# Kernel tuning notes

Measured on AMD Instinct MI355X. Metric: run time of the kernel, lower is better.

Reference implementation:

```python
import jax, jax.numpy as jnp
import numpy as np

B, H1, H2, D, V1 = 4, 512, 640, 640, 1025  # V1 = vocab_size + 1 (blank)
T, U = 256, 128


def setup_inputs() -> dict:
    key = jax.random.key(0)
    ks = jax.random.split(key, 8)
    s = lambda fan_in: 1.0 / np.sqrt(fan_in)
    return {
        "encoder_outputs": jax.random.normal(ks[0], (B, H1, T), jnp.float32),
        "predictor_outputs": jax.random.normal(ks[1], (B, H2, U), jnp.float32),
        # Linear weights stored as [in, out]
        "W_enc": jax.random.uniform(ks[2], (H1, D), jnp.float32, -s(H1), s(H1)),
        "b_enc": jax.random.uniform(ks[3], (D,), jnp.float32, -s(H1), s(H1)),
        "W_pred": jax.random.uniform(ks[4], (H2, D), jnp.float32, -s(H2), s(H2)),
        "b_pred": jax.random.uniform(ks[5], (D,), jnp.float32, -s(H2), s(H2)),
        "W_out": jax.random.uniform(ks[6], (D, V1), jnp.float32, -s(D), s(D)),
        "b_out": jax.random.uniform(ks[7], (V1,), jnp.float32, -s(D), s(D)),
    }


def reference(encoder_outputs, predictor_outputs, W_enc, b_enc, W_pred, b_pred, W_out, b_out):
    # transpose(1,2): [B,H1,T] -> [B,T,H1], [B,H2,U] -> [B,U,H2], fused into einsum
    f = jnp.einsum("bht,hd->btd", encoder_outputs, W_enc) + b_enc   # [B,T,D]
    g = jnp.einsum("bhu,hd->bud", predictor_outputs, W_pred) + b_pred  # [B,U,D]
    h = jax.nn.relu(f[:, :, None, :] + g[:, None, :, :])            # [B,T,U,D]
    logits = jnp.einsum("btud,dv->btuv", h, W_out) + b_out          # [B,T,U,V+1]
    return jax.nn.log_softmax(logits, axis=-1)
```

## Files before the change

### kernel.cpp

```cpp
#include <hip/hip_runtime.h>
#include <hip/hip_bf16.h>

#define Bb 4
#define Tt 256
#define Uu 128
#define H1 512
#define H2 640
#define Dd 640
#define V1c 1025

typedef __bf16 bf16x8 __attribute__((ext_vector_type(8)));
typedef unsigned short ushort8 __attribute__((ext_vector_type(8)));
typedef unsigned short ushort4v __attribute__((ext_vector_type(4)));
typedef float floatx4 __attribute__((ext_vector_type(4)));

static __device__ __forceinline__ unsigned short f2bf(float x) {
    union { float f; unsigned u; } a; a.f = x;
    unsigned r = a.u + 0x7fffu + ((a.u >> 16) & 1u);
    return (unsigned short)(r >> 16);
}
static __device__ __forceinline__ float bf2f(unsigned short x) {
    union { unsigned u; float f; } a; a.u = ((unsigned)x) << 16; return a.f;
}

__global__ __launch_bounds__(640) void prep(const float* __restrict__ enc,
                                            const float* __restrict__ Wenc,
                                            const float* __restrict__ benc,
                                            float* __restrict__ f,
                                            const float* __restrict__ pred,
                                            const float* __restrict__ Wpred,
                                            const float* __restrict__ bpred,
                                            float* __restrict__ g,
                                            const float* __restrict__ Wout,
                                            unsigned short* __restrict__ Wb2,
                                            float* __restrict__ wtail) {
    __shared__ __align__(16) float sh[640 * 8];
    const int tid = threadIdx.x;

    if (blockIdx.x < 192) {
        const bool isF = blockIdx.x < 128;
        const float* in   = isF ? enc : pred;
        const float* W    = isF ? Wenc : Wpred;
        const float* bias = isF ? benc : bpred;
        float* out        = isF ? f : g;
        const int H    = isF ? H1 : H2;
        const int Tdim = isF ? Tt : Uu;
        const int blk  = isF ? (int)blockIdx.x : (int)blockIdx.x - 128;
        const int tBlocks = Tdim >> 3;
        const int b  = blk / tBlocks;
        const int t0 = (blk % tBlocks) << 3;
        const float* inB = in + (size_t)b * H * Tdim + t0;

        for (int h = tid; h < H; h += 640) {
            float4 v0 = *(const float4*)(inB + (size_t)h * Tdim);
            float4 v1 = *(const float4*)(inB + (size_t)h * Tdim + 4);
            *(float4*)(&sh[h * 8])     = v0;
            *(float4*)(&sh[h * 8 + 4]) = v1;
        }
        __syncthreads();

        const int d = tid;
        float acc[8];
        #pragma unroll
        for (int j = 0; j < 8; ++j) acc[j] = 0.f;
        #pragma unroll 4
        for (int h = 0; h < H; ++h) {
            float w = W[(size_t)h * Dd + d];
            float4 s0 = *(const float4*)(&sh[h * 8]);
            float4 s1 = *(const float4*)(&sh[h * 8 + 4]);
            acc[0] += s0.x * w; acc[1] += s0.y * w; acc[2] += s0.z * w; acc[3] += s0.w * w;
            acc[4] += s1.x * w; acc[5] += s1.y * w; acc[6] += s1.z * w; acc[7] += s1.w * w;
        }
        float bv = bias[d];
        float* o = out + ((size_t)b * Tdim + t0) * Dd + d;
        #pragma unroll
        for (int j = 0; j < 8; ++j) o[(size_t)j * Dd] = acc[j] + bv;
    } else {
        float (*tile)[129] = (float(*)[129])sh;
        const int blk2 = blockIdx.x - 192;
        const int w = blk2 / 20;
        const int db = blk2 % 20;

        for (int idx = tid; idx < 4096; idx += 640) {
            int d_loc = idx >> 7;
            int v_loc = idx & 127;
            tile[d_loc][v_loc] = Wout[(size_t)(db * 32 + d_loc) * V1c + w * 128 + v_loc];
        }
        __syncthreads();

        if (tid < 512) {
            int gidx = tid;
            int nt  = gidx >> 6;
            int rem = gidx & 63;
            int l15 = rem >> 2;
            int lg  = rem & 3;
            int v_loc = nt * 16 + l15;
            ushort8 pk;
            #pragma unroll
            for (int j = 0; j < 8; ++j) pk[j] = f2bf(tile[lg * 8 + j][v_loc]);
            *(ushort8*)(Wb2 + (size_t)w * 81920 + db * 4096 + gidx * 8) = pk;
        }
        if (blk2 == 0 && tid < Dd) wtail[tid] = Wout[(size_t)tid * V1c + 1024];
    }
}

__global__ __launch_bounds__(512, 2) void joint_main(const float* __restrict__ f,
                                                     const float* __restrict__ g,
                                                     const unsigned short* __restrict__ Wb2,
                                                     const float* __restrict__ wtail,
                                                     const float* __restrict__ b_out,
                                                     float* __restrict__ out) {
    __shared__ __align__(16) union UU {
        unsigned short hlds[2 * 64 * 328];
        float sOut[16 * 1025];
    } u;
    __shared__ float wtld[640];
    __shared__ float sPart[8 * 64];
    __shared__ float sRed[64];
    __shared__ float sTail[64];

    const int tid = threadIdx.x;
    const int l = tid & 63;
    const int w = tid >> 6;
    const int l15 = l & 15;
    const int lg = l >> 4;

    const int blk = blockIdx.x;
    const int uhalf = blk & 1;
    const int t = (blk >> 1) & 255;
    const int b = blk >> 9;
    const int u0 = uhalf * 64;
    const size_t fbase = ((size_t)b * Tt + t) * Dd;
    const size_t gbase = ((size_t)b * Uu + u0) * Dd;
    const size_t rowbase = (size_t)(b * Tt + t) * Uu + u0;

    for (int i = tid; i < Dd; i += 512) wtld[i] = wtail[i];

    floatx4 acc[4][8];
    #pragma unroll
    for (int i = 0; i < 4; ++i)
        #pragma unroll
        for (int j = 0; j < 8; ++j) acc[i][j] = (floatx4){0.f, 0.f, 0.f, 0.f};

    const unsigned short* __restrict__ bbase = Wb2 + (size_t)w * 81920 + (l15 * 32 + lg * 8);
    float tailAcc = 0.f;
    const int srow = w * 8 + (l >> 3);
    const int ssub = l & 7;

    {
        const int row = tid >> 3;
        const float* frow = f + fbase;
        const float* grow = g + gbase + (size_t)row * Dd;
        #pragma unroll
        for (int j = 0; j < 20; ++j) {
            int c4 = (tid & 7) + 8 * j;
            int d = c4 * 4;
            int half = (j >= 10) ? 1 : 0;
            int cloc = c4 - half * 80;
            float4 fv = *(const float4*)(frow + d);
            float4 gv = *(const float4*)(grow + d);
            float h0 = fv.x + gv.x; h0 = h0 > 0.f ? h0 : 0.f;
            float h1 = fv.y + gv.y; h1 = h1 > 0.f ? h1 : 0.f;
            float h2 = fv.z + gv.z; h2 = h2 > 0.f ? h2 : 0.f;
            float h3 = fv.w + gv.w; h3 = h3 > 0.f ? h3 : 0.f;
            ushort4v pk;
            pk.x = f2bf(h0); pk.y = f2bf(h1); pk.z = f2bf(h2); pk.w = f2bf(h3);
            *(ushort4v*)(&u.hlds[half * 20992 + row * 328 + cloc * 4]) = pk;
        }
    }
    __syncthreads();

    {
        ushort8 Bbuf[2][8];
        #pragma unroll
        for (int nt = 0; nt < 8; ++nt)
            Bbuf[0][nt] = *(const ushort8*)(bbase + nt * 512);
        #pragma unroll
        for (int ksg = 0; ksg < 20; ++ksg) {
            if (ksg < 19) {
                #pragma unroll
                for (int nt = 0; nt < 8; ++nt)
                    Bbuf[(ksg + 1) & 1][nt] =
                        *(const ushort8*)(bbase + (ksg + 1) * 4096 + nt * 512);
            }
            const int bufo = (ksg >= 10) ? 20992 : 0;
            const int ks = (ksg >= 10) ? (ksg - 10) : ksg;
            bf16x8 afrag[4];
            #pragma unroll
            for (int mt = 0; mt < 4; ++mt) {
                ushort8 av = *(const ushort8*)(&u.hlds[bufo + (mt * 16 + l15) * 328 + ks * 32 + lg * 8]);
                afrag[mt] = __builtin_bit_cast(bf16x8, av);
            }
            #pragma unroll
            for (int nt = 0; nt < 8; ++nt) {
                bf16x8 bfrag = __builtin_bit_cast(bf16x8, Bbuf[ksg & 1][nt]);
                #pragma unroll
                for (int mt = 0; mt < 4; ++mt) {
                    acc[mt][nt] = __builtin_amdgcn_mfma_f32_16x16x32_bf16(
                        afrag[mt], bfrag, acc[mt][nt], 0, 0, 0);
                }
            }
        }
    }

    #pragma unroll
    for (int j = 0; j < 20; ++j) {
        int c4 = ssub + 8 * j;
        int half = (j >= 10) ? 1 : 0;
        int cloc = c4 - half * 80;
        ushort4v hv = *(const ushort4v*)(&u.hlds[half * 20992 + srow * 328 + cloc * 4]);
        float4 wv = *(const float4*)(&wtld[c4 * 4]);
        tailAcc += bf2f(hv.x) * wv.x + bf2f(hv.y) * wv.y +
                   bf2f(hv.z) * wv.z + bf2f(hv.w) * wv.w;
    }

    tailAcc += __shfl_xor(tailAcc, 1);
    tailAcc += __shfl_xor(tailAcc, 2);
    tailAcc += __shfl_xor(tailAcc, 4);
    if (ssub == 0) sTail[srow] = tailAcc + b_out[1024];

    #pragma unroll
    for (int nt = 0; nt < 8; ++nt) {
        float bo = b_out[w * 128 + nt * 16 + l15];
        #pragma unroll
        for (int mt = 0; mt < 4; ++mt)
            #pragma unroll
            for (int r = 0; r < 4; ++r) acc[mt][nt][r] += bo;
    }

    #pragma unroll
    for (int mt = 0; mt < 4; ++mt) {
        #pragma unroll
        for (int r = 0; r < 4; ++r) {
            float m = acc[mt][0][r];
            #pragma unroll
            for (int nt = 1; nt < 8; ++nt) m = fmaxf(m, acc[mt][nt][r]);
            #pragma unroll
            for (int msk = 1; msk < 16; msk <<= 1) m = fmaxf(m, __shfl_xor(m, msk));
            if (l15 == 0) sPart[w * 64 + mt * 16 + lg * 4 + r] = m;
        }
    }
    __syncthreads();
    if (tid < 64) {
        float m = sTail[tid];
        #pragma unroll
        for (int ww = 0; ww < 8; ++ww) m = fmaxf(m, sPart[ww * 64 + tid]);
        sRed[tid] = m;
    }
    __syncthreads();

    #pragma unroll
    for (int mt = 0; mt < 4; ++mt) {
        #pragma unroll
        for (int r = 0; r < 4; ++r) {
            int row = mt * 16 + lg * 4 + r;
            float mx = sRed[row];
            float sv = 0.f;
            #pragma unroll
            for (int nt = 0; nt < 8; ++nt) sv += __expf(acc[mt][nt][r] - mx);
            #pragma unroll
            for (int msk = 1; msk < 16; msk <<= 1) sv += __shfl_xor(sv, msk);
            if (l15 == 0) sPart[w * 64 + row] = sv;
        }
    }
    __syncthreads();
    if (tid < 64) {
        float mx = sRed[tid];
        float sv = __expf(sTail[tid] - mx);
        #pragma unroll
        for (int ww = 0; ww < 8; ++ww) sv += sPart[ww * 64 + tid];
        sRed[tid] = mx + logf(sv);
    }
    __syncthreads();

    #pragma unroll
    for (int grp = 0; grp < 4; ++grp) {
        #pragma unroll
        for (int nt = 0; nt < 8; ++nt) {
            #pragma unroll
            for (int r = 0; r < 4; ++r) {
                u.sOut[(lg * 4 + r) * 1025 + w * 128 + nt * 16 + l15] =
                    acc[grp][nt][r] - sRed[grp * 16 + lg * 4 + r];
            }
        }
        if (tid < 16) u.sOut[tid * 1025 + 1024] = sTail[grp * 16 + tid] - sRed[grp * 16 + tid];
        __syncthreads();
        float* outp = out + (rowbase + grp * 16) * (size_t)V1c;
        #pragma unroll
        for (int k = 0; k < 8; ++k) {
            int i4 = tid + 512 * k;
            *(floatx4*)(outp + 4 * i4) = *(const floatx4*)(&u.sOut[4 * i4]);
        }
        if (tid < 4) {
            int i4 = tid + 4096;
            *(floatx4*)(outp + 4 * i4) = *(const floatx4*)(&u.sOut[4 * i4]);
        }
        __syncthreads();
    }
}

extern "C" void kernel_launch(void* const* d_in, const int* in_sizes, int n_in,
                              void* d_out, int out_size, void* d_ws, size_t ws_size,
                              hipStream_t stream) {
    const float* enc   = (const float*)d_in[0];
    const float* pred  = (const float*)d_in[1];
    const float* Wenc  = (const float*)d_in[2];
    const float* benc  = (const float*)d_in[3];
    const float* Wpred = (const float*)d_in[4];
    const float* bpred = (const float*)d_in[5];
    const float* Wout  = (const float*)d_in[6];
    const float* bout  = (const float*)d_in[7];

    float* f = (float*)d_ws;
    float* g = f + (size_t)Bb * Tt * Dd;
    unsigned short* Wb2 = (unsigned short*)(g + (size_t)Bb * Uu * Dd);
    float* wtail = (float*)(Wb2 + 8 * 81920);

    prep<<<352, 640, 0, stream>>>(enc, Wenc, benc, f, pred, Wpred, bpred, g,
                                  Wout, Wb2, wtail);
    joint_main<<<Bb * Tt * 2, 512, 0, stream>>>(f, g, Wb2, wtail, bout, (float*)d_out);
}
```

Measured before the change: 424.5 us.

## Switch joint GEMM to 32x32x16 MFMA with 16 waves and nontemporal stores

```diff
diff --git a/kernel.cpp b/kernel.cpp
--- a/kernel.cpp
+++ b/kernel.cpp
@@ -13,6 +13,7 @@
 typedef unsigned short ushort8 __attribute__((ext_vector_type(8)));
 typedef unsigned short ushort4v __attribute__((ext_vector_type(4)));
 typedef float floatx4 __attribute__((ext_vector_type(4)));
+typedef float floatx16 __attribute__((ext_vector_type(16)));
 
 static __device__ __forceinline__ unsigned short f2bf(float x) {
     union { float f; unsigned u; } a; a.f = x;
@@ -32,7 +33,7 @@
                                             const float* __restrict__ bpred,
                                             float* __restrict__ g,
                                             const float* __restrict__ Wout,
-                                            unsigned short* __restrict__ Wb2,
+                                            unsigned short* __restrict__ Wb3,
                                             float* __restrict__ wtail) {
     __shared__ __align__(16) float sh[640 * 8];
     const int tid = threadIdx.x;
@@ -78,38 +79,41 @@
     } else {
         float (*tile)[129] = (float(*)[129])sh;
         const int blk2 = blockIdx.x - 192;
-        const int w = blk2 / 20;
-        const int db = blk2 % 20;
-
-        for (int idx = tid; idx < 4096; idx += 640) {
-            int d_loc = idx >> 7;
-            int v_loc = idx & 127;
-            tile[d_loc][v_loc] = Wout[(size_t)(db * 32 + d_loc) * V1c + w * 128 + v_loc];
+        const int cg = blk2 / 40;
+        const int ks = blk2 % 40;
+
+        if (tid < 512) {
+            #pragma unroll
+            for (int i = 0; i < 4; ++i) {
+                int idx = tid + 512 * i;
+                int d_loc = idx >> 7;
+                int v_loc = idx & 127;
+                tile[d_loc][v_loc] = Wout[(size_t)(ks * 16 + d_loc) * V1c + cg * 128 + v_loc];
+            }
         }
         __syncthreads();
 
-        if (tid < 512) {
-            int gidx = tid;
-            int nt  = gidx >> 6;
-            int rem = gidx & 63;
-            int l15 = rem >> 2;
-            int lg  = rem & 3;
-            int v_loc = nt * 16 + l15;
+        if (tid < 256) {
+            int ct  = tid >> 6;
+            int rem = tid & 63;
+            int l31 = rem >> 1;
+            int lh  = rem & 1;
+            int v_loc = ct * 32 + l31;
             ushort8 pk;
             #pragma unroll
-            for (int j = 0; j < 8; ++j) pk[j] = f2bf(tile[lg * 8 + j][v_loc]);
-            *(ushort8*)(Wb2 + (size_t)w * 81920 + db * 4096 + gidx * 8) = pk;
+            for (int j = 0; j < 8; ++j) pk[j] = f2bf(tile[lh * 8 + j][v_loc]);
+            *(ushort8*)(Wb3 + (size_t)cg * 81920 + ks * 2048 + tid * 8) = pk;
         }
         if (blk2 == 0 && tid < Dd) wtail[tid] = Wout[(size_t)tid * V1c + 1024];
     }
 }
 
-__global__ __launch_bounds__(512, 2) void joint_main(const float* __restrict__ f,
-                                                     const float* __restrict__ g,
-                                                     const unsigned short* __restrict__ Wb2,
-                                                     const float* __restrict__ wtail,
-                                                     const float* __restrict__ b_out,
-                                                     float* __restrict__ out) {
+__global__ __launch_bounds__(1024) void joint_main(const float* __restrict__ f,
+                                                   const float* __restrict__ g,
+                                                   const unsigned short* __restrict__ Wb3,
+                                                   const float* __restrict__ wtail,
+                                                   const float* __restrict__ b_out,
+                                                   float* __restrict__ out) {
     __shared__ __align__(16) union UU {
         unsigned short hlds[2 * 64 * 328];
         float sOut[16 * 1025];
@@ -122,8 +126,10 @@
     const int tid = threadIdx.x;
     const int l = tid & 63;
     const int w = tid >> 6;
-    const int l15 = l & 15;
-    const int lg = l >> 4;
+    const int rg = w >> 3;
+    const int cg = w & 7;
+    const int l31 = l & 31;
+    const int lh = l >> 5;
 
     const int blk = blockIdx.x;
     const int uhalf = blk & 1;
@@ -134,28 +140,28 @@
     const size_t gbase = ((size_t)b * Uu + u0) * Dd;
     const size_t rowbase = (size_t)(b * Tt + t) * Uu + u0;
 
-    for (int i = tid; i < Dd; i += 512) wtld[i] = wtail[i];
-
-    floatx4 acc[4][8];
+    if (tid < Dd) wtld[tid] = wtail[tid];
+
+    floatx16 acc[4];
     #pragma unroll
-    for (int i = 0; i < 4; ++i)
-        #pragma unroll
-        for (int j = 0; j < 8; ++j) acc[i][j] = (floatx4){0.f, 0.f, 0.f, 0.f};
-
-    const unsigned short* __restrict__ bbase = Wb2 + (size_t)w * 81920 + (l15 * 32 + lg * 8);
+    for (int ct = 0; ct < 4; ++ct)
+        #pragma unroll
+        for (int r = 0; r < 16; ++r) acc[ct][r] = 0.f;
+
+    const unsigned short* __restrict__ bbase = Wb3 + (size_t)cg * 81920 + (l31 * 16 + lh * 8);
     float tailAcc = 0.f;
-    const int srow = w * 8 + (l >> 3);
-    const int ssub = l & 7;
+    const int srow = tid >> 4;
+    const int ssub = tid & 15;
 
     {
-        const int row = tid >> 3;
+        const int row = tid >> 4;
         const float* frow = f + fbase;
         const float* grow = g + gbase + (size_t)row * Dd;
         #pragma unroll
-        for (int j = 0; j < 20; ++j) {
-            int c4 = (tid & 7) + 8 * j;
+        for (int j = 0; j < 10; ++j) {
+            int c4 = (tid & 15) + 16 * j;
             int d = c4 * 4;
-            int half = (j >= 10) ? 1 : 0;
+            int half = (j >= 5) ? 1 : 0;
             int cloc = c4 - half * 80;
             float4 fv = *(const float4*)(frow + d);
             float4 gv = *(const float4*)(grow + d);
@@ -171,96 +177,97 @@
     __syncthreads();
 
     {
-        ushort8 Bbuf[2][8];
-        #pragma unroll
-        for (int nt = 0; nt < 8; ++nt)
-            Bbuf[0][nt] = *(const ushort8*)(bbase + nt * 512);
-        #pragma unroll
-        for (int ksg = 0; ksg < 20; ++ksg) {
-            if (ksg < 19) {
+        const int arow = (rg * 32 + l31) * 328 + lh * 8;
+        ushort8 Bbuf[2][4];
+        #pragma unroll
+        for (int ct = 0; ct < 4; ++ct)
+            Bbuf[0][ct] = *(const ushort8*)(bbase + ct * 512);
+        #pragma unroll
+        for (int ks = 0; ks < 40; ++ks) {
+            if (ks < 39) {
                 #pragma unroll
-                for (int nt = 0; nt < 8; ++nt)
-                    Bbuf[(ksg + 1) & 1][nt] =
-                        *(const ushort8*)(bbase + (ksg + 1) * 4096 + nt * 512);
-            }
-            const int bufo = (ksg >= 10) ? 20992 : 0;
-            const int ks = (ksg >= 10) ? (ksg - 10) : ksg;
-            bf16x8 afrag[4];
-            #pragma unroll
-            for (int mt = 0; mt < 4; ++mt) {
-                ushort8 av = *(const ushort8*)(&u.hlds[bufo + (mt * 16 + l15) * 328 + ks * 32 + lg * 8]);
-                afrag[mt] = __builtin_bit_cast(bf16x8, av);
-            }
-            #pragma unroll
-            for (int nt = 0; nt < 8; ++nt) {
-                bf16x8 bfrag = __builtin_bit_cast(bf16x8, Bbuf[ksg & 1][nt]);
-                #pragma unroll
-                for (int mt = 0; mt < 4; ++mt) {
-                    acc[mt][nt] = __builtin_amdgcn_mfma_f32_16x16x32_bf16(
-                        afrag[mt], bfrag, acc[mt][nt], 0, 0, 0);
-                }
+                for (int ct = 0; ct < 4; ++ct)
+                    Bbuf[(ks + 1) & 1][ct] =
+                        *(const ushort8*)(bbase + (ks + 1) * 2048 + ct * 512);
+            }
+            const int bufo = (ks >= 20) ? 20992 : 0;
+            const int kk = (ks >= 20) ? (ks - 20) : ks;
+            ushort8 av = *(const ushort8*)(&u.hlds[bufo + arow + kk * 16]);
+            bf16x8 afrag = __builtin_bit_cast(bf16x8, av);
+            #pragma unroll
+            for (int ct = 0; ct < 4; ++ct) {
+                bf16x8 bfrag = __builtin_bit_cast(bf16x8, Bbuf[ks & 1][ct]);
+                acc[ct] = __builtin_amdgcn_mfma_f32_32x32x16_bf16(afrag, bfrag, acc[ct], 0, 0, 0);
             }
         }
     }
 
     #pragma unroll
-    for (int j = 0; j < 20; ++j) {
-        int c4 = ssub + 8 * j;
-        int half = (j >= 10) ? 1 : 0;
+    for (int j = 0; j < 10; ++j) {
+        int c4 = ssub + 16 * j;
+        int half = (c4 >= 80) ? 1 : 0;
         int cloc = c4 - half * 80;
         ushort4v hv = *(const ushort4v*)(&u.hlds[half * 20992 + srow * 328 + cloc * 4]);
         float4 wv = *(const float4*)(&wtld[c4 * 4]);
         tailAcc += bf2f(hv.x) * wv.x + bf2f(hv.y) * wv.y +
                    bf2f(hv.z) * wv.z + bf2f(hv.w) * wv.w;
     }
-
     tailAcc += __shfl_xor(tailAcc, 1);
     tailAcc += __shfl_xor(tailAcc, 2);
     tailAcc += __shfl_xor(tailAcc, 4);
+    tailAcc += __shfl_xor(tailAcc, 8);
     if (ssub == 0) sTail[srow] = tailAcc + b_out[1024];
 
     #pragma unroll
-    for (int nt = 0; nt < 8; ++nt) {
-        float bo = b_out[w * 128 + nt * 16 + l15];
-        #pragma unroll
-        for (int mt = 0; mt < 4; ++mt)
-            #pragma unroll
-            for (int r = 0; r < 4; ++r) acc[mt][nt][r] += bo;
-    }
-
-    #pragma unroll
-    for (int mt = 0; mt < 4; ++mt) {
-        #pragma unroll
-        for (int r = 0; r < 4; ++r) {
-            float m = acc[mt][0][r];
-            #pragma unroll
-            for (int nt = 1; nt < 8; ++nt) m = fmaxf(m, acc[mt][nt][r]);
-            #pragma unroll
-            for (int msk = 1; msk < 16; msk <<= 1) m = fmaxf(m, __shfl_xor(m, msk));
-            if (l15 == 0) sPart[w * 64 + mt * 16 + lg * 4 + r] = m;
+    for (int ct = 0; ct < 4; ++ct) {
+        float bo = b_out[cg * 128 + ct * 32 + l31];
+        #pragma unroll
+        for (int r = 0; r < 16; ++r) acc[ct][r] += bo;
+    }
+
+
+    {
+        float m[16];
+        #pragma unroll
+        for (int r = 0; r < 16; ++r) {
+            m[r] = fmaxf(fmaxf(acc[0][r], acc[1][r]), fmaxf(acc[2][r], acc[3][r]));
+            #pragma unroll
+            for (int msk = 1; msk < 32; msk <<= 1) m[r] = fmaxf(m[r], __shfl_xor(m[r], msk));
+        }
+        if (l31 == 0) {
+            #pragma unroll
+            for (int r = 0; r < 16; ++r) {
+                int rowloc = (r & 3) + 8 * (r >> 2) + 4 * lh;
+                sPart[cg * 64 + rg * 32 + rowloc] = m[r];
+            }
         }
     }
     __syncthreads();
     if (tid < 64) {
         float m = sTail[tid];
         #pragma unroll
-        for (int ww = 0; ww < 8; ++ww) m = fmaxf(m, sPart[ww * 64 + tid]);
+        for (int c = 0; c < 8; ++c) m = fmaxf(m, sPart[c * 64 + tid]);
         sRed[tid] = m;
     }
     __syncthreads();
 
-    #pragma unroll
-    for (int mt = 0; mt < 4; ++mt) {
-        #pragma unroll
-        for (int r = 0; r < 4; ++r) {
-            int row = mt * 16 + lg * 4 + r;
-            float mx = sRed[row];
-            float sv = 0.f;
-            #pragma unroll
-            for (int nt = 0; nt < 8; ++nt) sv += __expf(acc[mt][nt][r] - mx);
-            #pragma unroll
-            for (int msk = 1; msk < 16; msk <<= 1) sv += __shfl_xor(sv, msk);
-            if (l15 == 0) sPart[w * 64 + row] = sv;
+    {
+        float sv[16];
+        #pragma unroll
+        for (int r = 0; r < 16; ++r) {
+            int rowloc = (r & 3) + 8 * (r >> 2) + 4 * lh;
+            float mx = sRed[rg * 32 + rowloc];
+            sv[r] = __expf(acc[0][r] - mx) + __expf(acc[1][r] - mx) +
+                    __expf(acc[2][r] - mx) + __expf(acc[3][r] - mx);
+            #pragma unroll
+            for (int msk = 1; msk < 32; msk <<= 1) sv[r] += __shfl_xor(sv[r], msk);
+        }
+        if (l31 == 0) {
+            #pragma unroll
+            for (int r = 0; r < 16; ++r) {
+                int rowloc = (r & 3) + 8 * (r >> 2) + 4 * lh;
+                sPart[cg * 64 + rg * 32 + rowloc] = sv[r];
+            }
         }
     }
     __syncthreads();
@@ -268,32 +275,39 @@
         float mx = sRed[tid];
         float sv = __expf(sTail[tid] - mx);
         #pragma unroll
-        for (int ww = 0; ww < 8; ++ww) sv += sPart[ww * 64 + tid];
+        for (int c = 0; c < 8; ++c) sv += sPart[c * 64 + tid];
         sRed[tid] = mx + logf(sv);
     }
     __syncthreads();
 
     #pragma unroll
     for (int grp = 0; grp < 4; ++grp) {
-        #pragma unroll
-        for (int nt = 0; nt < 8; ++nt) {
-            #pragma unroll
-            for (int r = 0; r < 4; ++r) {
-                u.sOut[(lg * 4 + r) * 1025 + w * 128 + nt * 16 + l15] =
-                    acc[grp][nt][r] - sRed[grp * 16 + lg * 4 + r];
+        if (rg == (grp >> 1)) {
+            const int rb = (grp & 1) * 8;
+            #pragma unroll
+            for (int rr = 0; rr < 8; ++rr) {
+                int r = rb + rr;
+                int row16 = (r & 3) + 8 * ((r >> 2) & 1) + 4 * lh;
+                float lse = sRed[grp * 16 + row16];
+                #pragma unroll
+                for (int ct = 0; ct < 4; ++ct) {
+                    u.sOut[row16 * 1025 + cg * 128 + ct * 32 + l31] = acc[ct][r] - lse;
+                }
             }
         }
         if (tid < 16) u.sOut[tid * 1025 + 1024] = sTail[grp * 16 + tid] - sRed[grp * 16 + tid];
         __syncthreads();
         float* outp = out + (rowbase + grp * 16) * (size_t)V1c;
         #pragma unroll
-        for (int k = 0; k < 8; ++k) {
-            int i4 = tid + 512 * k;
-            *(floatx4*)(outp + 4 * i4) = *(const floatx4*)(&u.sOut[4 * i4]);
+        for (int k = 0; k < 4; ++k) {
+            int i4 = tid + 1024 * k;
+            floatx4 v = *(const floatx4*)(&u.sOut[4 * i4]);
+            __builtin_nontemporal_store(v, (floatx4*)(outp + 4 * i4));
         }
         if (tid < 4) {
             int i4 = tid + 4096;
-            *(floatx4*)(outp + 4 * i4) = *(const floatx4*)(&u.sOut[4 * i4]);
+            floatx4 v = *(const floatx4*)(&u.sOut[4 * i4]);
+            __builtin_nontemporal_store(v, (floatx4*)(outp + 4 * i4));
         }
         __syncthreads();
     }
@@ -313,10 +327,10 @@
 
     float* f = (float*)d_ws;
     float* g = f + (size_t)Bb * Tt * Dd;
-    unsigned short* Wb2 = (unsigned short*)(g + (size_t)Bb * Uu * Dd);
-    float* wtail = (float*)(Wb2 + 8 * 81920);
-
-    prep<<<352, 640, 0, stream>>>(enc, Wenc, benc, f, pred, Wpred, bpred, g,
-                                  Wout, Wb2, wtail);
-    joint_main<<<Bb * Tt * 2, 512, 0, stream>>>(f, g, Wb2, wtail, bout, (float*)d_out);
-}
+    unsigned short* Wb3 = (unsigned short*)(g + (size_t)Bb * Uu * Dd);
+    float* wtail = (float*)(Wb3 + 8 * 81920);
+
+    prep<<<512, 640, 0, stream>>>(enc, Wenc, benc, f, pred, Wpred, bpred, g,
+                                  Wout, Wb3, wtail);
+    joint_main<<<Bb * Tt * 2, 1024, 0, stream>>>(f, g, Wb3, wtail, bout, (float*)d_out);
+}
```

After: 375.9 us (median of 2 runs). 1.13x faster.

## Use online softmax merge and direct nontemporal stores instead of LDS-staged output

Applied to the files above, without the earlier changes.

```diff
diff --git a/kernel.cpp b/kernel.cpp
--- a/kernel.cpp
+++ b/kernel.cpp
@@ -110,12 +110,10 @@
                                                      const float* __restrict__ wtail,
                                                      const float* __restrict__ b_out,
                                                      float* __restrict__ out) {
-    __shared__ __align__(16) union UU {
-        unsigned short hlds[2 * 64 * 328];
-        float sOut[16 * 1025];
-    } u;
+    __shared__ __align__(16) unsigned short hlds[2 * 64 * 328];
     __shared__ float wtld[640];
-    __shared__ float sPart[8 * 64];
+    __shared__ float sPartM[8 * 64];
+    __shared__ float sPartS[8 * 64];
     __shared__ float sRed[64];
     __shared__ float sTail[64];
 
@@ -165,7 +163,7 @@
             float h3 = fv.w + gv.w; h3 = h3 > 0.f ? h3 : 0.f;
             ushort4v pk;
             pk.x = f2bf(h0); pk.y = f2bf(h1); pk.z = f2bf(h2); pk.w = f2bf(h3);
-            *(ushort4v*)(&u.hlds[half * 20992 + row * 328 + cloc * 4]) = pk;
+            *(ushort4v*)(&hlds[half * 20992 + row * 328 + cloc * 4]) = pk;
         }
     }
     __syncthreads();
@@ -188,7 +186,7 @@
             bf16x8 afrag[4];
             #pragma unroll
             for (int mt = 0; mt < 4; ++mt) {
-                ushort8 av = *(const ushort8*)(&u.hlds[bufo + (mt * 16 + l15) * 328 + ks * 32 + lg * 8]);
+                ushort8 av = *(const ushort8*)(&hlds[bufo + (mt * 16 + l15) * 328 + ks * 32 + lg * 8]);
                 afrag[mt] = __builtin_bit_cast(bf16x8, av);
             }
             #pragma unroll
@@ -208,7 +206,7 @@
         int c4 = ssub + 8 * j;
         int half = (j >= 10) ? 1 : 0;
         int cloc = c4 - half * 80;
-        ushort4v hv = *(const ushort4v*)(&u.hlds[half * 20992 + srow * 328 + cloc * 4]);
+        ushort4v hv = *(const ushort4v*)(&hlds[half * 20992 + srow * 328 + cloc * 4]);
         float4 wv = *(const float4*)(&wtld[c4 * 4]);
         tailAcc += bf2f(hv.x) * wv.x + bf2f(hv.y) * wv.y +
                    bf2f(hv.z) * wv.z + bf2f(hv.w) * wv.w;
@@ -232,20 +230,31 @@
     for (int mt = 0; mt < 4; ++mt) {
         #pragma unroll
         for (int r = 0; r < 4; ++r) {
+            int row = mt * 16 + lg * 4 + r;
             float m = acc[mt][0][r];
             #pragma unroll
             for (int nt = 1; nt < 8; ++nt) m = fmaxf(m, acc[mt][nt][r]);
             #pragma unroll
             for (int msk = 1; msk < 16; msk <<= 1) m = fmaxf(m, __shfl_xor(m, msk));
-            if (l15 == 0) sPart[w * 64 + mt * 16 + lg * 4 + r] = m;
+            float sv = 0.f;
+            #pragma unroll
+            for (int nt = 0; nt < 8; ++nt) sv += __expf(acc[mt][nt][r] - m);
+            #pragma unroll
+            for (int msk = 1; msk < 16; msk <<= 1) sv += __shfl_xor(sv, msk);
+            if (l15 == 0) { sPartM[w * 64 + row] = m; sPartS[w * 64 + row] = sv; }
         }
     }
     __syncthreads();
+
     if (tid < 64) {
-        float m = sTail[tid];
-        #pragma unroll
-        for (int ww = 0; ww < 8; ++ww) m = fmaxf(m, sPart[ww * 64 + tid]);
-        sRed[tid] = m;
+        float tl = sTail[tid];
+        float m = tl;
+        #pragma unroll
+        for (int c = 0; c < 8; ++c) m = fmaxf(m, sPartM[c * 64 + tid]);
+        float sv = __expf(tl - m);
+        #pragma unroll
+        for (int c = 0; c < 8; ++c) sv += sPartS[c * 64 + tid] * __expf(sPartM[c * 64 + tid] - m);
+        sRed[tid] = m + logf(sv);
     }
     __syncthreads();
 
@@ -253,49 +262,18 @@
     for (int mt = 0; mt < 4; ++mt) {
         #pragma unroll
         for (int r = 0; r < 4; ++r) {
-            int row = mt * 16 + lg * 4 + r;
-            float mx = sRed[row];
-            float sv = 0.f;
-            #pragma unroll
-            for (int nt = 0; nt < 8; ++nt) sv += __expf(acc[mt][nt][r] - mx);
-            #pragma unroll
-            for (int msk = 1; msk < 16; msk <<= 1) sv += __shfl_xor(sv, msk);
-            if (l15 == 0) sPart[w * 64 + row] = sv;
-        }
-    }
-    __syncthreads();
+            const int row = mt * 16 + lg * 4 + r;
+            const float lse = sRed[row];
+            float* rowp = out + (rowbase + row) * (size_t)V1c + w * 128 + l15;
+            #pragma unroll
+            for (int nt = 0; nt < 8; ++nt) {
+                __builtin_nontemporal_store(acc[mt][nt][r] - lse, rowp + nt * 16);
+            }
+        }
+    }
     if (tid < 64) {
-        float mx = sRed[tid];
-        float sv = __expf(sTail[tid] - mx);
-        #pragma unroll
-        for (int ww = 0; ww < 8; ++ww) sv += sPart[ww * 64 + tid];
-        sRed[tid] = mx + logf(sv);
-    }
-    __syncthreads();
-
-    #pragma unroll
-    for (int grp = 0; grp < 4; ++grp) {
-        #pragma unroll
-        for (int nt = 0; nt < 8; ++nt) {
-            #pragma unroll
-            for (int r = 0; r < 4; ++r) {
-                u.sOut[(lg * 4 + r) * 1025 + w * 128 + nt * 16 + l15] =
-                    acc[grp][nt][r] - sRed[grp * 16 + lg * 4 + r];
-            }
-        }
-        if (tid < 16) u.sOut[tid * 1025 + 1024] = sTail[grp * 16 + tid] - sRed[grp * 16 + tid];
-        __syncthreads();
-        float* outp = out + (rowbase + grp * 16) * (size_t)V1c;
-        #pragma unroll
-        for (int k = 0; k < 8; ++k) {
-            int i4 = tid + 512 * k;
-            *(floatx4*)(outp + 4 * i4) = *(const floatx4*)(&u.sOut[4 * i4]);
-        }
-        if (tid < 4) {
-            int i4 = tid + 4096;
-            *(floatx4*)(outp + 4 * i4) = *(const floatx4*)(&u.sOut[4 * i4]);
-        }
-        __syncthreads();
+        __builtin_nontemporal_store(sTail[tid] - sRed[tid],
+                                    out + (rowbase + tid) * (size_t)V1c + 1024);
     }
 }
 
```

Result: no change. 422.7 us (-0.4%).
